# Performance work log

Hardware: AMD Instinct MI355X
Metric: run time of the kernel (lower is better)

## Reference

```python
import jax, jax.numpy as jnp
import numpy as np

EPS = 1e-5
T = 8          # n_segment
PATCH = 3      # corr_size


def _bn(x, g, b):
    # eval-mode BatchNorm with running_mean=0, running_var=1 (init values)
    shape = (1, -1) + (1,) * (x.ndim - 2)
    inv = 1.0 / jnp.sqrt(1.0 + EPS)
    return x * (g * inv).reshape(shape) + b.reshape(shape)


def setup_inputs() -> dict:
    key = jax.random.key(0)
    k1, k2, k3 = jax.random.split(key, 3)
    nt, c, h, w = 64, 256, 56, 56
    cr = 64  # c // reduction, reduction = 4
    return {
        "x": jax.random.normal(k1, (nt, c, h, w), dtype=jnp.float32),
        "conv21_w": jax.random.normal(k2, (cr, c), dtype=jnp.float32) * 0.05,
        "bn21_g": jnp.ones((cr,), jnp.float32),
        "bn21_b": jnp.zeros((cr,), jnp.float32),
        "bn22_g": jnp.ones((PATCH * PATCH,), jnp.float32),
        "bn22_b": jnp.zeros((PATCH * PATCH,), jnp.float32),
        "conv22_w": jax.random.normal(k3, (c, PATCH * PATCH), dtype=jnp.float32) * 0.05,
        "bn23_g": jnp.ones((c,), jnp.float32),
        "bn23_b": jnp.zeros((c,), jnp.float32),
    }


def reference(x, conv21_w, bn21_g, bn21_b, bn22_g, bn22_b, conv22_w, bn23_g, bn23_b):
    nt, c, h, w = x.shape
    n = nt // T
    cr = conv21_w.shape[0]
    residual = x

    # (n, c, T, h, w)
    xv = x.reshape(n, T, c, h, w).transpose(0, 2, 1, 3, 4)
    # conv21: 1x1x1 Conv3d c -> cr, no bias
    y = jnp.einsum('oc,ncthw->nothw', conv21_w, xv)
    y = jax.nn.relu(_bn(y, bn21_g, bn21_b))

    # temporally shifted copy: frame t paired with frame min(t+1, T-1)
    idx = jnp.minimum(jnp.arange(1, T + 1), T - 1)
    y2 = y[:, :, idx, :, :]

    # flatten back to (nt, cr, h, w)
    x1 = y.transpose(0, 2, 1, 3, 4).reshape(nt, cr, h, w)
    x2 = y2.transpose(0, 2, 1, 3, 4).reshape(nt, cr, h, w)

    # SpatialCorrelationSampler(kernel_size=1, patch_size=3): zero-padded
    # displacements (dy, dx) in {-1,0,1}^2, dot product over channels.
    pad = PATCH // 2
    x2p = jnp.pad(x2, ((0, 0), (0, 0), (pad, pad), (pad, pad)))
    cv = jnp.stack(
        [jnp.einsum('nchw,nchw->nhw', x1, x2p[:, :, dy:dy + h, dx:dx + w])
         for dy in range(PATCH) for dx in range(PATCH)],
        axis=1,
    ) / cr  # (nt, 9, h, w), divided by c // (reduction * corr_group)

    cv = jax.nn.relu(_bn(cv, bn22_g, bn22_b))
    # conv22: 1x1 Conv2d 9 -> c, no bias
    out = jnp.einsum('ok,nkhw->nohw', conv22_w, cv)
    out = _bn(out, bn23_g, bn23_b) + residual
    return jax.nn.relu(out)
```

## Files before the change

kernel.cpp:

```cpp
#include <hip/hip_runtime.h>

#define HW     3136
#define WIDTH  56
#define C      256
#define CR     64
#define NT     64
#define TT     8
#define PW     64
#define PH     58
#define YPLANE (PH*PW)
#define YBYTES ((size_t)NT * CR * YPLANE * 2)

#define BN_INV 0.9999950000374997f

typedef __attribute__((ext_vector_type(8))) short short8;
typedef __attribute__((ext_vector_type(8))) unsigned short ushort8;
typedef __attribute__((ext_vector_type(4))) float f32x4;
typedef __attribute__((ext_vector_type(2))) float f32x2;

static __device__ __forceinline__ float relu(float v) { return fmaxf(v, 0.0f); }
static __device__ __forceinline__ float bf2f(unsigned short u) {
    return __builtin_bit_cast(float, (unsigned)u << 16);
}
static __device__ __forceinline__ unsigned short f2bf(float f) {
    unsigned u = __builtin_bit_cast(unsigned, f);
    unsigned r = (u + 0x7FFFu + ((u >> 16) & 1u)) >> 16;
    return (unsigned short)r;
}
static __device__ __forceinline__ unsigned pack2(float a, float b) {
    return (unsigned)f2bf(a) | ((unsigned)f2bf(b) << 16);
}

static __device__ __forceinline__ void halo_zero(int nt, int tid,
                                                 unsigned short* __restrict__ y) {
    const int ch = tid >> 2, part = tid & 3;
    unsigned short* pl = y + ((size_t)nt * CR + ch) * YPLANE;
    if (part == 0) {
        ushort8 z = (ushort8)0;
#pragma unroll
        for (int j = 0; j < 8; ++j) *(ushort8*)(pl + j * 8) = z;
    } else if (part == 1) {
        ushort8 z = (ushort8)0;
        unsigned short* q = pl + 57 * PW;
#pragma unroll
        for (int j = 0; j < 8; ++j) *(ushort8*)(q + j * 8) = z;
    } else if (part == 2) {
        for (int r = 1; r <= 28; ++r) {
            unsigned short* q = pl + r * PW + 57;
#pragma unroll
            for (int j = 0; j < 8; ++j) q[j] = 0;
        }
    } else {
        for (int r = 29; r <= 56; ++r) {
            unsigned short* q = pl + r * PW + 57;
#pragma unroll
            for (int j = 0; j < 8; ++j) q[j] = 0;
        }
        pl[PW] = 0;
    }
}

__global__ __launch_bounds__(256, 2) void k1_mfma(const float* __restrict__ x,
                                                  const float* __restrict__ w21,
                                                  const float* __restrict__ g,
                                                  const float* __restrict__ bb,
                                                  unsigned short* __restrict__ y) {
    const int blk = blockIdx.x;
    const int tid = threadIdx.x;
    if (blk >= 784) { halo_zero(blk - 784, tid, y); return; }
    const int bs = (blk & 7) * 98 + (blk >> 3);

    __shared__ unsigned short Alds[64][264];
    __shared__ unsigned short Blds[4][64][40];

    const int lane = tid & 63;
    const int wv   = tid >> 6;
    const int gq   = bs / 49;
    const int s    = bs - gq * 49;
    const int p0   = s * 64;
    const int nt   = __builtin_amdgcn_readfirstlane(gq * 4 + wv);

    {
        const int o  = tid >> 2;
        const int cb = (tid & 3) * 64;
        const float* wp = w21 + o * C + cb;
        unsigned short* ap = &Alds[o][cb];
#pragma unroll
        for (int j = 0; j < 8; ++j) {
            f32x4 lo = *(const f32x4*)(wp + j * 8);
            f32x4 hi = *(const f32x4*)(wp + j * 8 + 4);
            union { unsigned d[4]; short8 v; } pk;
            pk.d[0] = pack2(lo.x, lo.y); pk.d[1] = pack2(lo.z, lo.w);
            pk.d[2] = pack2(hi.x, hi.y); pk.d[3] = pack2(hi.z, hi.w);
            *(short8*)(ap + j * 8) = pk.v;
        }
    }
    __syncthreads();

    const float* xw = x + (size_t)nt * (C * HW) + p0 + lane;
    unsigned short (*Bw)[40] = Blds[wv];

    f32x4 acc[4][4];
#pragma unroll
    for (int nb = 0; nb < 4; ++nb)
#pragma unroll
        for (int mb = 0; mb < 4; ++mb) acc[nb][mb] = (f32x4)0.0f;

    const int frow = lane & 15;
    const int fk8  = (lane >> 4) * 8;

    float buf[2][32];
#pragma unroll
    for (int j = 0; j < 32; ++j) buf[0][j] = xw[(size_t)j * HW];

#pragma unroll
    for (int ks = 0; ks < 8; ++ks) {
        const int cur = ks & 1;
        if (ks < 7) {
            const float* xn = xw + (size_t)((ks + 1) * 32) * HW;
#pragma unroll
            for (int j = 0; j < 32; ++j) buf[cur ^ 1][j] = xn[(size_t)j * HW];
        }
#pragma unroll
        for (int q = 0; q < 4; ++q) {
            union { unsigned d[4]; short8 v; } pk;
#pragma unroll
            for (int jj = 0; jj < 4; ++jj)
                pk.d[jj] = pack2(buf[cur][q * 8 + 2 * jj], buf[cur][q * 8 + 2 * jj + 1]);
            *(short8*)&Bw[lane][q * 8] = pk.v;
        }
        short8 bfrag[4], afrag[4];
#pragma unroll
        for (int nb = 0; nb < 4; ++nb)
            bfrag[nb] = *(const short8*)&Bw[nb * 16 + frow][fk8];
#pragma unroll
        for (int mb = 0; mb < 4; ++mb)
            afrag[mb] = *(const short8*)&Alds[mb * 16 + frow][ks * 32 + fk8];
#pragma unroll
        for (int nb = 0; nb < 4; ++nb)
#pragma unroll
            for (int mb = 0; mb < 4; ++mb)
                acc[nb][mb] = __builtin_amdgcn_mfma_f32_16x16x32_bf16(
                    afrag[mb], bfrag[nb], acc[nb][mb], 0, 0, 0);
    }

    unsigned short* ybase = y + (size_t)nt * CR * YPLANE;
    const int rbase = (lane >> 4) * 4;
#pragma unroll
    for (int nb = 0; nb < 4; ++nb) {
        const int p = p0 + nb * 16 + frow;
        const int r = p / WIDTH;
        const int c = p - r * WIDTH;
        const int pidx = (r + 1) * PW + (c + 1);
#pragma unroll
        for (int mb = 0; mb < 4; ++mb)
#pragma unroll
            for (int rr = 0; rr < 4; ++rr) {
                int o = mb * 16 + rbase + rr;
                float v = relu(fmaf(acc[nb][mb][rr], g[o] * BN_INV, bb[o]));
                ybase[(size_t)o * YPLANE + pidx] = f2bf(v);
            }
    }
}

__global__ __launch_bounds__(256) void k2_corr(const unsigned short* __restrict__ y,
                                               const float* __restrict__ g,
                                               const float* __restrict__ bb,
                                               float* __restrict__ cv) {
    const int bs = (blockIdx.x & 7) * 49 + (blockIdx.x >> 3);
    int gt   = bs * 256 + threadIdx.x;
    int h    = gt & 3;
    int task = gt >> 2;
    int nt   = task / 392;
    int rm   = task - nt * 392;
    int r    = rm / 7;
    int cg   = rm - r * 7;
    int c0   = cg * 8;
    int nt2  = ((nt & (TT - 1)) < TT - 1) ? nt + 1 : nt;

    const unsigned short* y1 = y + ((size_t)nt * CR + h * 16) * YPLANE
                                 + (size_t)(r + 1) * PW + c0;
    const unsigned short* y2 = y + ((size_t)nt2 * CR + h * 16) * YPLANE
                                 + (size_t)r * PW + c0;

    float acc[9][8];
#pragma unroll
    for (int k = 0; k < 9; ++k)
#pragma unroll
        for (int px = 0; px < 8; ++px) acc[k][px] = 0.0f;

#pragma unroll 2
    for (int ch = 0; ch < 16; ++ch) {
        const unsigned short* p1 = y1 + (size_t)ch * YPLANE;
        ushort8 a8 = *(const ushort8*)p1;
        unsigned at = *(const unsigned*)(p1 + 8);
        float a[8];
#pragma unroll
        for (int j = 0; j < 7; ++j) a[j] = bf2f(a8[j + 1]);
        a[7] = bf2f((unsigned short)(at & 0xffffu));

        const unsigned short* p2 = y2 + (size_t)ch * YPLANE;
#pragma unroll
        for (int dy = 0; dy < 3; ++dy) {
            const unsigned short* pr = p2 + dy * PW;
            ushort8 b8 = *(const ushort8*)pr;
            unsigned bt = *(const unsigned*)(pr + 8);
            float w[10];
#pragma unroll
            for (int j = 0; j < 8; ++j) w[j] = bf2f(b8[j]);
            w[8] = bf2f((unsigned short)(bt & 0xffffu));
            w[9] = bf2f((unsigned short)(bt >> 16));
#pragma unroll
            for (int dx = 0; dx < 3; ++dx) {
                int k = dy * 3 + dx;
#pragma unroll
                for (int px = 0; px < 8; ++px)
                    acc[k][px] = fmaf(a[px], w[px + dx], acc[k][px]);
            }
        }
    }

#pragma unroll
    for (int k = 0; k < 9; ++k)
#pragma unroll
        for (int px = 0; px < 8; ++px) {
            float v = acc[k][px];
            v += __shfl_xor(v, 1);
            v += __shfl_xor(v, 2);
            acc[k][px] = v;
        }

    if (h == 0) {
        float* cp = cv + (size_t)nt * 9 * HW + r * WIDTH + c0;
        const float rcr = 1.0f / CR;
#pragma unroll
        for (int k = 0; k < 9; ++k) {
            float sc = g[k] * BN_INV, bv = bb[k];
            f32x4 lo, hi;
            lo.x = relu(fmaf(acc[k][0] * rcr, sc, bv));
            lo.y = relu(fmaf(acc[k][1] * rcr, sc, bv));
            lo.z = relu(fmaf(acc[k][2] * rcr, sc, bv));
            lo.w = relu(fmaf(acc[k][3] * rcr, sc, bv));
            hi.x = relu(fmaf(acc[k][4] * rcr, sc, bv));
            hi.y = relu(fmaf(acc[k][5] * rcr, sc, bv));
            hi.z = relu(fmaf(acc[k][6] * rcr, sc, bv));
            hi.w = relu(fmaf(acc[k][7] * rcr, sc, bv));
            *(f32x4*)(cp + (size_t)k * HW)     = lo;
            *(f32x4*)(cp + (size_t)k * HW + 4) = hi;
        }
    }
}

__global__ __launch_bounds__(256) void k3_conv22(const float* __restrict__ cv,
                                                 const float* __restrict__ w2,
                                                 const float* __restrict__ g,
                                                 const float* __restrict__ bb,
                                                 const float* __restrict__ x,
                                                 float* __restrict__ out) {
    const int bs = (blockIdx.x & 7) * 49 + (blockIdx.x >> 3);
    int gt = bs * 256 + threadIdx.x;
    int nt = gt / 1568;
    int p2 = (gt - nt * 1568) * 2;

    const float* cp = cv + (size_t)nt * 9 * HW + p2;
    float cvx[9], cvy[9];
#pragma unroll
    for (int k = 0; k < 9; ++k) {
        f32x2 v = *(const f32x2*)(cp + (size_t)k * HW);
        cvx[k] = v.x; cvy[k] = v.y;
    }

    const float* xp = x   + (size_t)nt * (C * HW) + p2;
    float*       op = out + (size_t)nt * (C * HW) + p2;

#pragma unroll 8
    for (int o = 0; o < C; ++o) {
        const float* wr = w2 + o * 9;
        f32x2 xr = *(const f32x2*)(xp + (size_t)o * HW);
        float sx = 0.0f, sy = 0.0f;
#pragma unroll
        for (int k = 0; k < 9; ++k) {
            float wv = wr[k];
            sx = fmaf(wv, cvx[k], sx);
            sy = fmaf(wv, cvy[k], sy);
        }
        float sc = g[o] * BN_INV, bv = bb[o];
        f32x2 rv;
        rv.x = relu(fmaf(sx, sc, bv) + xr.x);
        rv.y = relu(fmaf(sy, sc, bv) + xr.y);
        *(f32x2*)(op + (size_t)o * HW) = rv;
    }
}

extern "C" void kernel_launch(void* const* d_in, const int* in_sizes, int n_in,
                              void* d_out, int out_size, void* d_ws, size_t ws_size,
                              hipStream_t stream) {
    const float* x   = (const float*)d_in[0];
    const float* w21 = (const float*)d_in[1];
    const float* g21 = (const float*)d_in[2];
    const float* b21 = (const float*)d_in[3];
    const float* g22 = (const float*)d_in[4];
    const float* b22 = (const float*)d_in[5];
    const float* w22 = (const float*)d_in[6];
    const float* g23 = (const float*)d_in[7];
    const float* b23 = (const float*)d_in[8];
    float* out = (float*)d_out;

    unsigned short* yb  = (unsigned short*)d_ws;
    float*          cvb = (float*)((char*)d_ws + YBYTES);

    k1_mfma  <<<848, 256, 0, stream>>>(x, w21, g21, b21, yb);
    k2_corr  <<<392, 256, 0, stream>>>(yb, g22, b22, cvb);
    k3_conv22<<<392, 256, 0, stream>>>(cvb, w22, g23, b23, x, out);
}
```

Before: 188.8 us.

## Retile conv21 MFMA kernel with shared double-buffered B tile and prepacked bf16 weights

Adds a small kernel that converts conv21 weights to bf16 once, so the GEMM blocks read A fragments straight from global memory instead of each block repacking them into LDS. The main GEMM kernel now covers 256 pixels per block with a block-shared, XOR-swizzled, double-buffered LDS B tile filled by vectorised float4 loads, plus a separate tail launch for the last 64 pixels. The block-index swizzle in the correlation and conv22 kernels is dropped. The cost is two extra launches and more registers per thread for the larger accumulator tile, and occupancy may change because the launch-bounds hint is removed.

```diff
diff --git a/kernel.cpp b/kernel.cpp
--- a/kernel.cpp
+++ b/kernel.cpp
@@ -10,6 +10,7 @@
 #define PH     58
 #define YPLANE (PH*PW)
 #define YBYTES ((size_t)NT * CR * YPLANE * 2)
+#define CVBYTES ((size_t)NT * 9 * HW * 4)
 
 #define BN_INV 0.9999950000374997f
 
@@ -29,6 +30,12 @@
 }
 static __device__ __forceinline__ unsigned pack2(float a, float b) {
     return (unsigned)f2bf(a) | ((unsigned)f2bf(b) << 16);
+}
+
+__global__ __launch_bounds__(256) void k0_cvt_w(const float* __restrict__ w,
+                                                unsigned short* __restrict__ wbf) {
+    int i = blockIdx.x * 256 + threadIdx.x;
+    wbf[i] = f2bf(w[i]);
 }
 
 static __device__ __forceinline__ void halo_zero(int nt, int tid,
@@ -60,95 +67,109 @@
     }
 }
 
-__global__ __launch_bounds__(256, 2) void k1_mfma(const float* __restrict__ x,
-                                                  const float* __restrict__ w21,
-                                                  const float* __restrict__ g,
-                                                  const float* __restrict__ bb,
-                                                  unsigned short* __restrict__ y) {
-    const int blk = blockIdx.x;
-    const int tid = threadIdx.x;
-    if (blk >= 784) { halo_zero(blk - 784, tid, y); return; }
-    const int bs = (blk & 7) * 98 + (blk >> 3);
-
-    __shared__ unsigned short Alds[64][264];
-    __shared__ unsigned short Blds[4][64][40];
-
+template<int TP>
+__global__ __launch_bounds__(256) void k1_mfma(const float* __restrict__ x,
+                                               const unsigned short* __restrict__ wbf,
+                                               const float* __restrict__ g,
+                                               const float* __restrict__ bb,
+                                               unsigned short* __restrict__ y) {
+    constexpr int NB = TP / 64;
+    constexpr int NQ = TP / 4;
+    __shared__ unsigned short Bl[2][NQ][136];
+
+    const int tid  = threadIdx.x;
     const int lane = tid & 63;
     const int wv   = tid >> 6;
-    const int gq   = bs / 49;
-    const int s    = bs - gq * 49;
-    const int p0   = s * 64;
-    const int nt   = __builtin_amdgcn_readfirstlane(gq * 4 + wv);
-
-    {
-        const int o  = tid >> 2;
-        const int cb = (tid & 3) * 64;
-        const float* wp = w21 + o * C + cb;
-        unsigned short* ap = &Alds[o][cb];
-#pragma unroll
-        for (int j = 0; j < 8; ++j) {
-            f32x4 lo = *(const f32x4*)(wp + j * 8);
-            f32x4 hi = *(const f32x4*)(wp + j * 8 + 4);
-            union { unsigned d[4]; short8 v; } pk;
-            pk.d[0] = pack2(lo.x, lo.y); pk.d[1] = pack2(lo.z, lo.w);
-            pk.d[2] = pack2(hi.x, hi.y); pk.d[3] = pack2(hi.z, hi.w);
-            *(short8*)(ap + j * 8) = pk.v;
-        }
-    }
+
+    int nt, px0;
+    if (TP == 256) {
+        if (blockIdx.x >= 768) { halo_zero(blockIdx.x - 768, tid, y); return; }
+        nt = blockIdx.x / 12; px0 = (blockIdx.x % 12) * 256;
+    } else {
+        nt = blockIdx.x; px0 = 3072;
+    }
+
+    const int p4 = tid & (NQ - 1);
+    const int c8 = tid / NQ;
+    const bool active = (TP == 256) ? true : (c8 < 4);
+
+    const float* xbase = x + (size_t)nt * (C * HW) + px0 + 4 * p4;
+    const int frow = lane & 15;
+    const int hi   = lane >> 4;
+    const unsigned short* abase = wbf + frow * C + hi * 8;
+
+    f32x4 acc[NB][4];
+#pragma unroll
+    for (int nb = 0; nb < NB; ++nb)
+#pragma unroll
+        for (int mb = 0; mb < 4; ++mb) acc[nb][mb] = (f32x4)0.0f;
+
+    f32x4  xq[8];
+    short8 afr[2][4];
+
+#define LOADB(KS)                                                          \
+    if (active) {                                                          \
+        const float* _p = xbase + (size_t)((KS) * 32 + c8 * 8) * HW;       \
+        _Pragma("unroll")                                                  \
+        for (int j = 0; j < 8; ++j) xq[j] = *(const f32x4*)(_p + (size_t)j * HW); \
+    }
+
+#define LOADA(KS, DST)                                                     \
+    _Pragma("unroll")                                                      \
+    for (int mb = 0; mb < 4; ++mb)                                         \
+        (DST)[mb] = *(const short8*)(abase + mb * 16 * C + (KS) * 32);
+
+#define WRITEB(BUF)                                                        \
+    if (active) {                                                          \
+        _Pragma("unroll")                                                  \
+        for (int i = 0; i < 4; ++i) {                                      \
+            union { unsigned d[4]; short8 v; } pk;                         \
+            pk.d[0] = pack2(xq[0][i], xq[1][i]);                           \
+            pk.d[1] = pack2(xq[2][i], xq[3][i]);                           \
+            pk.d[2] = pack2(xq[4][i], xq[5][i]);                           \
+            pk.d[3] = pack2(xq[6][i], xq[7][i]);                           \
+            *(short8*)&Bl[BUF][p4][i * 32 + ((c8 ^ i) & 3) * 8] = pk.v;    \
+        }                                                                  \
+    }
+
+    LOADB(0)
+    LOADA(0, afr[0])
+    WRITEB(0)
     __syncthreads();
 
-    const float* xw = x + (size_t)nt * (C * HW) + p0 + lane;
-    unsigned short (*Bw)[40] = Blds[wv];
-
-    f32x4 acc[4][4];
-#pragma unroll
-    for (int nb = 0; nb < 4; ++nb)
-#pragma unroll
-        for (int mb = 0; mb < 4; ++mb) acc[nb][mb] = (f32x4)0.0f;
-
-    const int frow = lane & 15;
-    const int fk8  = (lane >> 4) * 8;
-
-    float buf[2][32];
-#pragma unroll
-    for (int j = 0; j < 32; ++j) buf[0][j] = xw[(size_t)j * HW];
-
 #pragma unroll
     for (int ks = 0; ks < 8; ++ks) {
-        const int cur = ks & 1;
+        const int cb = ks & 1;
         if (ks < 7) {
-            const float* xn = xw + (size_t)((ks + 1) * 32) * HW;
-#pragma unroll
-            for (int j = 0; j < 32; ++j) buf[cur ^ 1][j] = xn[(size_t)j * HW];
-        }
-#pragma unroll
-        for (int q = 0; q < 4; ++q) {
-            union { unsigned d[4]; short8 v; } pk;
-#pragma unroll
-            for (int jj = 0; jj < 4; ++jj)
-                pk.d[jj] = pack2(buf[cur][q * 8 + 2 * jj], buf[cur][q * 8 + 2 * jj + 1]);
-            *(short8*)&Bw[lane][q * 8] = pk.v;
-        }
-        short8 bfrag[4], afrag[4];
-#pragma unroll
-        for (int nb = 0; nb < 4; ++nb)
-            bfrag[nb] = *(const short8*)&Bw[nb * 16 + frow][fk8];
-#pragma unroll
-        for (int mb = 0; mb < 4; ++mb)
-            afrag[mb] = *(const short8*)&Alds[mb * 16 + frow][ks * 32 + fk8];
-#pragma unroll
-        for (int nb = 0; nb < 4; ++nb)
+            LOADB(ks + 1)
+            LOADA(ks + 1, afr[cb ^ 1])
+        }
+        short8 bfrag[NB];
+#pragma unroll
+        for (int nb = 0; nb < NB; ++nb) {
+            const int pxl = wv * (TP / 4) + nb * 16 + frow;
+            bfrag[nb] = *(const short8*)
+                &Bl[cb][pxl >> 2][(pxl & 3) * 32 + ((hi ^ (pxl & 3)) & 3) * 8];
+        }
+#pragma unroll
+        for (int nb = 0; nb < NB; ++nb)
 #pragma unroll
             for (int mb = 0; mb < 4; ++mb)
                 acc[nb][mb] = __builtin_amdgcn_mfma_f32_16x16x32_bf16(
-                    afrag[mb], bfrag[nb], acc[nb][mb], 0, 0, 0);
-    }
+                    afr[cb][mb], bfrag[nb], acc[nb][mb], 0, 0, 0);
+        if (ks < 7) {
+            WRITEB(cb ^ 1)
+            __syncthreads();
+        }
+    }
+#undef LOADB
+#undef LOADA
+#undef WRITEB
 
     unsigned short* ybase = y + (size_t)nt * CR * YPLANE;
-    const int rbase = (lane >> 4) * 4;
-#pragma unroll
-    for (int nb = 0; nb < 4; ++nb) {
-        const int p = p0 + nb * 16 + frow;
+#pragma unroll
+    for (int nb = 0; nb < NB; ++nb) {
+        const int p = px0 + wv * (TP / 4) + nb * 16 + frow;
         const int r = p / WIDTH;
         const int c = p - r * WIDTH;
         const int pidx = (r + 1) * PW + (c + 1);
@@ -156,7 +177,7 @@
         for (int mb = 0; mb < 4; ++mb)
 #pragma unroll
             for (int rr = 0; rr < 4; ++rr) {
-                int o = mb * 16 + rbase + rr;
+                int o = mb * 16 + hi * 4 + rr;
                 float v = relu(fmaf(acc[nb][mb][rr], g[o] * BN_INV, bb[o]));
                 ybase[(size_t)o * YPLANE + pidx] = f2bf(v);
             }
@@ -167,8 +188,7 @@
                                                const float* __restrict__ g,
                                                const float* __restrict__ bb,
                                                float* __restrict__ cv) {
-    const int bs = (blockIdx.x & 7) * 49 + (blockIdx.x >> 3);
-    int gt   = bs * 256 + threadIdx.x;
+    int gt   = blockIdx.x * 256 + threadIdx.x;
     int h    = gt & 3;
     int task = gt >> 2;
     int nt   = task / 392;
@@ -257,8 +277,7 @@
                                                  const float* __restrict__ bb,
                                                  const float* __restrict__ x,
                                                  float* __restrict__ out) {
-    const int bs = (blockIdx.x & 7) * 49 + (blockIdx.x >> 3);
-    int gt = bs * 256 + threadIdx.x;
+    int gt = blockIdx.x * 256 + threadIdx.x;
     int nt = gt / 1568;
     int p2 = (gt - nt * 1568) * 2;
 
@@ -308,8 +327,11 @@
 
     unsigned short* yb  = (unsigned short*)d_ws;
     float*          cvb = (float*)((char*)d_ws + YBYTES);
-
-    k1_mfma  <<<848, 256, 0, stream>>>(x, w21, g21, b21, yb);
-    k2_corr  <<<392, 256, 0, stream>>>(yb, g22, b22, cvb);
-    k3_conv22<<<392, 256, 0, stream>>>(cvb, w22, g23, b23, x, out);
-}
+    unsigned short* wbf = (unsigned short*)((char*)d_ws + YBYTES + CVBYTES);
+
+    k0_cvt_w     <<<64,  256, 0, stream>>>(w21, wbf);
+    k1_mfma<256> <<<832, 256, 0, stream>>>(x, wbf, g21, b21, yb);
+    k1_mfma<64>  <<<64,  256, 0, stream>>>(x, wbf, g21, b21, yb);
+    k2_corr      <<<392, 256, 0, stream>>>(yb, g22, b22, cvb);
+    k3_conv22    <<<392, 256, 0, stream>>>(cvb, w22, g23, b23, x, out);
+}
```

New measurement: 195.7 us. 1.04x slower.
